# Kernel tuning notes

Hardware: AMD Instinct MI355X
Metric: run time of the kernel (lower is better)

## Reference

```python
import jax, jax.numpy as jnp
import numpy as np

B, S, D, H = 2, 2048, 2048, 16
HD = D // H
QMAX = 127.0  # 8-bit activation quant


def ste_round(x):
    # forward: round; backward: identity
    return x + jax.lax.stop_gradient(jnp.round(x) - x)


def bitlinear(x, w):
    """BitNet b1.58 linear: per-tensor ternary weights + per-token int8 activations.

    x: [..., in], w: [out, in] -> [..., out]
    """
    w_scale = jnp.maximum(jnp.mean(jnp.abs(w)), 1e-6)
    w_q = jnp.clip(ste_round(w / w_scale), -1.0, 1.0)          # ternary {-1,0,1}
    a_max = jnp.clip(jnp.max(jnp.abs(x), axis=-1, keepdims=True), 1e-8, None)
    x_q = jnp.clip(ste_round(x * (QMAX / a_max)), -QMAX, QMAX)  # int8 range
    y = jnp.einsum('bsi,oi->bso', x_q, w_q)
    return y * (w_scale * a_max / QMAX)


def setup_inputs() -> dict:
    key = jax.random.key(0)
    ks = jax.random.split(key, 5)
    std = 1.0 / np.sqrt(D)  # muP-style init from BitLinear
    return {
        'x': jax.random.normal(ks[0], (B, S, D), dtype=jnp.float32),
        'wq': jax.random.normal(ks[1], (D, D), dtype=jnp.float32) * std,
        'wk': jax.random.normal(ks[2], (D, D), dtype=jnp.float32) * std,
        'wv': jax.random.normal(ks[3], (D, D), dtype=jnp.float32) * std,
        'wo': jax.random.normal(ks[4], (D, D), dtype=jnp.float32) * std,
    }


def reference(x, wq, wk, wv, wo):
    q = bitlinear(x, wq).reshape(B, S, H, HD)
    k = bitlinear(x, wk).reshape(B, S, H, HD)
    v = bitlinear(x, wv).reshape(B, S, H, HD)
    scores = jnp.einsum('bqhd,bkhd->bhqk', q, k) / np.sqrt(HD)
    # causal mask
    causal = jnp.tril(jnp.ones((S, S), dtype=bool))
    scores = jnp.where(causal[None, None], scores, jnp.finfo(scores.dtype).min)
    attn = jax.nn.softmax(scores, axis=-1)
    ctx = jnp.einsum('bhqk,bkhd->bqhd', attn, v).reshape(B, S, D)
    return bitlinear(ctx, wo)
```

## Files before the change

kernel.cpp:

```cpp
#include <hip/hip_runtime.h>
#include <hip/hip_bf16.h>
#include <cstdint>
#include <cstddef>


#define BB 2
#define SS 2048
#define DD 2048
#define HH 16
#define HDD 128
#define MM (BB*SS)

typedef __attribute__((ext_vector_type(8))) short bf16x8;
typedef __attribute__((ext_vector_type(4))) float f32x4;
typedef __attribute__((ext_vector_type(16))) float f32x16;
typedef __attribute__((ext_vector_type(4))) int   i32x4;
typedef unsigned short u16;
typedef unsigned int   u32;
typedef unsigned char  u8;
typedef signed char    s8;

#define MFMA(a,b,c)   __builtin_amdgcn_mfma_f32_16x16x32_bf16(a,b,c,0,0,0)
#define MFMA32(a,b,c) __builtin_amdgcn_mfma_f32_32x32x16_bf16(a,b,c,0,0,0)
#define MFMAI8(a,b,c) __builtin_amdgcn_mfma_i32_16x16x64_i8(a,b,c,0,0,0)

static __device__ __forceinline__ u16 f2bf(float f) {
  u32 x = __float_as_uint(f);
  u32 r = x + 0x7fffu + ((x >> 16) & 1u);
  return (u16)(r >> 16);
}

static __device__ __forceinline__ void gl_lds16(const void* g, void* l) {
  __builtin_amdgcn_global_load_lds((const __attribute__((address_space(1))) void*)g,
                                   (__attribute__((address_space(3))) void*)l, 16, 0, 0);
}

__global__ void k_wabs_partial(const float* __restrict__ w0, const float* __restrict__ w1,
                               const float* __restrict__ w2, const float* __restrict__ w3,
                               double* __restrict__ part) {
  int m = blockIdx.x >> 8, blk = blockIdx.x & 255;
  const float* w = (m == 0) ? w0 : (m == 1) ? w1 : (m == 2) ? w2 : w3;
  const float* p = w + (size_t)blk * 16384;
  double s = 0.0;
  for (int i = threadIdx.x * 4; i < 16384; i += 1024) {
    float4 v = *(const float4*)(p + i);
    s += (double)fabsf(v.x) + (double)fabsf(v.y) + (double)fabsf(v.z) + (double)fabsf(v.w);
  }
  __shared__ double red[256];
  red[threadIdx.x] = s;
  __syncthreads();
  for (int off = 128; off > 0; off >>= 1) {
    if ((int)threadIdx.x < off) red[threadIdx.x] += red[threadIdx.x + off];
    __syncthreads();
  }
  if (threadIdx.x == 0) part[m * 256 + blk] = red[0];
}

__global__ void k_wscale_final(const double* __restrict__ part, float* __restrict__ scales) {
  int m = threadIdx.x;
  if (m < 4) {
    double s = 0.0;
    for (int i = 0; i < 256; i++) s += part[m * 256 + i];
    float v = (float)(s * (1.0 / 4194304.0));
    scales[m] = fmaxf(v, 1e-6f);
  }
}

__global__ void k_wquant(const float* __restrict__ w0, const float* __restrict__ w1,
                         const float* __restrict__ w2, const float* __restrict__ w3,
                         s8* __restrict__ wq, const float* __restrict__ scales) {
  int m = blockIdx.y;
  const float* w = (m == 0) ? w0 : (m == 1) ? w1 : (m == 2) ? w2 : w3;
  float ws = scales[m];
  size_t i = ((size_t)blockIdx.x * 256 + threadIdx.x) * 4;
  float4 v = *(const float4*)(w + i);
  s8 o[4];
  o[0] = (s8)(int)fminf(1.f, fmaxf(-1.f, rintf(v.x / ws)));
  o[1] = (s8)(int)fminf(1.f, fmaxf(-1.f, rintf(v.y / ws)));
  o[2] = (s8)(int)fminf(1.f, fmaxf(-1.f, rintf(v.z / ws)));
  o[3] = (s8)(int)fminf(1.f, fmaxf(-1.f, rintf(v.w / ws)));
  *(int*)(wq + (size_t)m * DD * DD + i) = *(const int*)o;
}

__global__ __launch_bounds__(256) void k_rowquant(const float* __restrict__ x, s8* __restrict__ xq,
                                                  float* __restrict__ amax) {
  int row = blockIdx.x, t = threadIdx.x;
  const float* p = x + (size_t)row * DD + t * 8;
  float4 v0 = *(const float4*)(p);
  float4 v1 = *(const float4*)(p + 4);
  float m = fmaxf(fmaxf(fmaxf(fabsf(v0.x), fabsf(v0.y)), fmaxf(fabsf(v0.z), fabsf(v0.w))),
                  fmaxf(fmaxf(fabsf(v1.x), fabsf(v1.y)), fmaxf(fabsf(v1.z), fabsf(v1.w))));
  m = fmaxf(m, __shfl_xor(m, 1));  m = fmaxf(m, __shfl_xor(m, 2));
  m = fmaxf(m, __shfl_xor(m, 4));  m = fmaxf(m, __shfl_xor(m, 8));
  m = fmaxf(m, __shfl_xor(m, 16)); m = fmaxf(m, __shfl_xor(m, 32));
  __shared__ float red[4];
  if ((t & 63) == 0) red[t >> 6] = m;
  __syncthreads();
  m = fmaxf(fmaxf(red[0], red[1]), fmaxf(red[2], red[3]));
  m = fmaxf(m, 1e-8f);
  if (t == 0) amax[row] = m;
  float s = 127.0f / m;
  s8 o[8];
  o[0] = (s8)(int)fminf(127.f, fmaxf(-127.f, rintf(v0.x * s)));
  o[1] = (s8)(int)fminf(127.f, fmaxf(-127.f, rintf(v0.y * s)));
  o[2] = (s8)(int)fminf(127.f, fmaxf(-127.f, rintf(v0.z * s)));
  o[3] = (s8)(int)fminf(127.f, fmaxf(-127.f, rintf(v0.w * s)));
  o[4] = (s8)(int)fminf(127.f, fmaxf(-127.f, rintf(v1.x * s)));
  o[5] = (s8)(int)fminf(127.f, fmaxf(-127.f, rintf(v1.y * s)));
  o[6] = (s8)(int)fminf(127.f, fmaxf(-127.f, rintf(v1.z * s)));
  o[7] = (s8)(int)fminf(127.f, fmaxf(-127.f, rintf(v1.w * s)));
  *(uint2*)(xq + (size_t)row * DD + t * 8) = *(const uint2*)o;
}

template<bool OB, int NBNL>
__global__ __launch_bounds__(512) void k_gemm(const s8* __restrict__ A, const s8* __restrict__ Bw,
                                              const float* __restrict__ amax,
                                              const float* __restrict__ scales, int sbase,
                                              void* __restrict__ outv) {
  __shared__ alignas(16) u8 Asm[2][128 * 128];
  __shared__ alignas(16) u8 Bsm[2][256 * 128];
  int id = blockIdx.x;
  int xcd = id & 7, kk = id >> 3;
  int bm = kk & 31, bn = xcd * NBNL + (kk >> 5);
  int t = threadIdx.x, w = t >> 6, l = t & 63;
  int wr = w >> 2, wc = w & 3;
  int l15 = l & 15, lh = l >> 4;
  int r0 = t >> 3;
  int c0 = ((t & 7) ^ (r0 & 7)) * 16;
  const s8* Ab = A  + (size_t)(bm * 128) * DD;
  const s8* Bb = Bw + (size_t)(bn * 256) * DD;

#define STG_A(tt) do { u8* d_ = &Asm[(tt) & 1][0];                                    \
    gl_lds16(Ab + (size_t)r0 * DD + (tt) * 128 + c0,        d_ + t * 16);             \
    gl_lds16(Ab + (size_t)(r0 + 64) * DD + (tt) * 128 + c0, d_ + (512 + t) * 16); } while (0)
#define STG_B(tt, h_) do { u8* d_ = &Bsm[(tt) & 1][(h_) * 16384];                     \
    gl_lds16(Bb + (size_t)((h_) * 128 + r0) * DD + (tt) * 128 + c0,        d_ + t * 16);\
    gl_lds16(Bb + (size_t)((h_) * 128 + r0 + 64) * DD + (tt) * 128 + c0,   d_ + (512 + t) * 16); } while (0)

  i32x4 acc[4][4] = {};
  STG_A(0); STG_B(0, 0); STG_B(0, 1); STG_B(1, 0);
  asm volatile("s_waitcnt vmcnt(2)" ::: "memory");
  asm volatile("s_barrier" ::: "memory");
  for (int kb = 0; kb < 16; kb++) {
    int b = kb & 1;
    const u8* Ac = &Asm[b][0];
    const u8* Bc = &Bsm[b][0];
    i32x4 af[4][2], bf[2][2];
    #pragma unroll
    for (int i = 0; i < 4; i++)
      #pragma unroll
      for (int ks = 0; ks < 2; ks++)
        af[i][ks] = *(const i32x4*)(Ac + (wr * 64 + i * 16 + l15) * 128 + (((ks * 4 + lh) ^ (l15 & 7)) * 16));
    #pragma unroll
    for (int j = 0; j < 2; j++)
      #pragma unroll
      for (int ks = 0; ks < 2; ks++)
        bf[j][ks] = *(const i32x4*)(Bc + ((wc + 4 * j) * 16 + l15) * 128 + (((ks * 4 + lh) ^ (l15 & 7)) * 16));
    if (kb + 1 < 16) { STG_A(kb + 1); STG_B(kb + 1, 1); }
    asm volatile("s_barrier" ::: "memory");
    asm volatile("s_waitcnt lgkmcnt(0)" ::: "memory");
    __builtin_amdgcn_sched_barrier(0);
    __builtin_amdgcn_s_setprio(1);
    #pragma unroll
    for (int ks = 0; ks < 2; ks++)
      #pragma unroll
      for (int i = 0; i < 4; i++)
        #pragma unroll
        for (int j = 0; j < 2; j++)
          acc[i][j] = MFMAI8(af[i][ks], bf[j][ks], acc[i][j]);
    __builtin_amdgcn_s_setprio(0);
    asm volatile("s_barrier" ::: "memory");
    i32x4 bg[2][2];
    #pragma unroll
    for (int j = 0; j < 2; j++)
      #pragma unroll
      for (int ks = 0; ks < 2; ks++)
        bg[j][ks] = *(const i32x4*)(Bc + ((wc + 4 * (2 + j)) * 16 + l15) * 128 + (((ks * 4 + lh) ^ (l15 & 7)) * 16));
    if (kb + 2 < 16) STG_B(kb + 2, 0);
    asm volatile("s_barrier" ::: "memory");
    asm volatile("s_waitcnt lgkmcnt(0)" ::: "memory");
    __builtin_amdgcn_sched_barrier(0);
    __builtin_amdgcn_s_setprio(1);
    #pragma unroll
    for (int ks = 0; ks < 2; ks++)
      #pragma unroll
      for (int i = 0; i < 4; i++)
        #pragma unroll
        for (int j = 0; j < 2; j++)
          acc[i][2 + j] = MFMAI8(af[i][ks], bg[j][ks], acc[i][2 + j]);
    __builtin_amdgcn_s_setprio(0);
    if (kb < 14) {
      asm volatile("s_waitcnt vmcnt(2)" ::: "memory");
      asm volatile("s_barrier" ::: "memory");
    } else if (kb == 14) {
      asm volatile("s_waitcnt vmcnt(0)" ::: "memory");
      asm volatile("s_barrier" ::: "memory");
    }
  }
#undef STG_A
#undef STG_B
  int mz = OB ? (bn >> 3) : 0;
  int lcol0 = OB ? ((bn & 7) * 256) : (bn * 256);
  float wsc = scales[sbase + mz];
  u16*   outb = (u16*)outv + (size_t)mz * MM * DD;
  float* outf = (float*)outv;
  #pragma unroll
  for (int i = 0; i < 4; i++) {
    int row0 = bm * 128 + wr * 64 + i * 16 + lh * 4;
    #pragma unroll
    for (int r = 0; r < 4; r++) {
      float sc = (wsc * amax[row0 + r]) / 127.0f;
      #pragma unroll
      for (int j = 0; j < 4; j++) {
        int col = lcol0 + (wc + 4 * j) * 16 + l15;
        float y = (float)acc[i][j][r] * sc;
        if (OB) outb[(size_t)(row0 + r) * DD + col] = f2bf(y);
        else    outf[(size_t)(row0 + r) * DD + col] = y;
      }
    }
  }
}

__global__ __launch_bounds__(256) void k_vtrans(const u16* __restrict__ v, u16* __restrict__ vt) {
  __shared__ u16 tile[64][72];
  int sb = blockIdx.x;
  int db = blockIdx.y;
  int bh = blockIdx.z;
  int b = bh >> 4, h = bh & 15;
  int t = threadIdx.x;
  int ls = t >> 2, ld0 = (t & 3) * 16;
  const u16* src = v + (size_t)(b * SS + sb * 64 + ls) * DD + h * HDD + db * 64 + ld0;
  *(int4*)(&tile[ls][ld0])     = *(const int4*)(src);
  *(int4*)(&tile[ls][ld0 + 8]) = *(const int4*)(src + 8);
  __syncthreads();
  int d = t >> 2, s0 = (t & 3) * 16;
  u16 tmp[16];
  #pragma unroll
  for (int k = 0; k < 16; k++) tmp[k] = tile[s0 + k][d];
  u16* dst = vt + (size_t)((bh * HDD) + db * 64 + d) * SS + sb * 64 + s0;
  *(int4*)(dst)     = *(const int4*)(tmp);
  *(int4*)(dst + 8) = *(const int4*)(tmp + 8);
}

__global__ __launch_bounds__(128) void k_attn(const u16* __restrict__ Q, const u16* __restrict__ K,
                                              const u16* __restrict__ VT, float* __restrict__ O) {
  __shared__ u16 Ks[64 * 128];
  __shared__ u16 Vs[128 * 64];
  __shared__ u16 Ps[2 * 32 * 64];
  int id = blockIdx.x;
  int bh = (id & 7) * 4 + ((id >> 3) & 3);
  int qt = 31 - (id >> 5);
  int b = bh >> 4, h = bh & 15;
  int t = threadIdx.x, w = t >> 6, l = t & 63;
  int l31 = l & 31, hi = l >> 5;
  int l15 = l & 15, lh = l >> 4;
  size_t base = (size_t)(b * SS) * DD + h * HDD;
  const u16* vtb = VT + (size_t)bh * HDD * SS;
  u16* Ptw = Ps + w * 2048;
  const float sc  = 0.08838834764831845f;
  const float sc2 = 0.12751944557270094f;
  int ksr[8], kso[8], vsr[8], vso[8];
  #pragma unroll
  for (int i = 0; i < 8; i++) {
    int s = i * 128 + t;
    ksr[i] = s >> 4; kso[i] = ((s & 15) ^ (ksr[i] & 15)) * 8;
    vsr[i] = s >> 3; vso[i] = ((s & 7) ^ (vsr[i] & 7)) * 8;
  }
  int qrow = qt * 64 + w * 32 + l31;
  bf16x8 qf[8];
  #pragma unroll
  for (int kt = 0; kt < 8; kt++)
    qf[kt] = *(const bf16x8*)(Q + base + (size_t)qrow * DD + kt * 16 + hi * 8);
  f32x4 cacc[2][8] = {};
  float mrun = -INFINITY, lrun = 0.f;
  for (int kb = 0; kb <= qt; kb++) {
    #pragma unroll
    for (int i = 0; i < 8; i++)
      gl_lds16(K + base + (size_t)(kb * 64 + ksr[i]) * DD + kso[i], Ks + (i * 128 + t) * 8);
    #pragma unroll
    for (int i = 0; i < 8; i++)
      gl_lds16(vtb + (size_t)vsr[i] * SS + kb * 64 + vso[i], Vs + (i * 128 + t) * 8);
    __syncthreads();
    f32x16 c0 = {}, c1 = {};
    #pragma unroll
    for (int kt = 0; kt < 8; kt++) {
      int sl = (((kt * 2 + hi) ^ (l31 & 15)) * 8);
      bf16x8 kf0 = *(const bf16x8*)(Ks + l31 * 128 + sl);
      bf16x8 kf1 = *(const bf16x8*)(Ks + (32 + l31) * 128 + sl);
      c0 = MFMA32(kf0, qf[kt], c0);
      c1 = MFMA32(kf1, qf[kt], c1);
    }
    if (kb == qt) {
      #pragma unroll
      for (int rg = 0; rg < 16; rg++) {
        int kv0 = kb * 64 + (rg & 3) + 8 * (rg >> 2) + 4 * hi;
        if (kv0 > qrow)      c0[rg] = -1e30f;
        if (kv0 + 32 > qrow) c1[rg] = -1e30f;
      }
    }
    float ta[16];
    #pragma unroll
    for (int rg = 0; rg < 16; rg++) ta[rg] = fmaxf(c0[rg], c1[rg]);
    #pragma unroll
    for (int off = 8; off > 0; off >>= 1)
      #pragma unroll
      for (int rg = 0; rg < 8; rg++)
        if (rg < off) ta[rg] = fmaxf(ta[rg], ta[rg + off]);
    float pmax = fmaxf(ta[0], __shfl_xor(ta[0], 32));
    if (__any(pmax - mrun > 90.50967f)) {
      float mnew = fmaxf(mrun, pmax);
      float alpha = __builtin_amdgcn_exp2f((mrun - mnew) * sc2);
      lrun *= alpha;
      #pragma unroll
      for (int m16 = 0; m16 < 2; m16++)
        #pragma unroll
        for (int r = 0; r < 4; r++) {
          float ar = __shfl(alpha, m16 * 16 + lh * 4 + r);
          #pragma unroll
          for (int n2 = 0; n2 < 8; n2++) cacc[m16][n2][r] *= ar;
        }
      mrun = mnew;
    }
    float msc2 = mrun * sc2;
    float ts[16];
    #pragma unroll
    for (int rg = 0; rg < 16; rg++) {
      float p0 = __builtin_amdgcn_exp2f(fmaf(c0[rg], sc2, -msc2)); c0[rg] = p0;
      float p1 = __builtin_amdgcn_exp2f(fmaf(c1[rg], sc2, -msc2)); c1[rg] = p1;
      ts[rg] = p0 + p1;
    }
    #pragma unroll
    for (int off = 8; off > 0; off >>= 1)
      #pragma unroll
      for (int rg = 0; rg < 8; rg++)
        if (rg < off) ts[rg] += ts[rg + off];
    lrun += ts[0] + __shfl_xor(ts[0], 32);
    #pragma unroll
    for (int q4 = 0; q4 < 4; q4++) {
      uint2 pk0, pk1;
      pk0.x = (u32)f2bf(c0[4 * q4 + 0]) | ((u32)f2bf(c0[4 * q4 + 1]) << 16);
      pk0.y = (u32)f2bf(c0[4 * q4 + 2]) | ((u32)f2bf(c0[4 * q4 + 3]) << 16);
      pk1.x = (u32)f2bf(c1[4 * q4 + 0]) | ((u32)f2bf(c1[4 * q4 + 1]) << 16);
      pk1.y = (u32)f2bf(c1[4 * q4 + 2]) | ((u32)f2bf(c1[4 * q4 + 3]) << 16);
      *(uint2*)(Ptw + l31 * 64 + ((q4 ^ (l31 & 7)) * 8 + 4 * hi))       = pk0;
      *(uint2*)(Ptw + l31 * 64 + (((4 + q4) ^ (l31 & 7)) * 8 + 4 * hi)) = pk1;
    }
    #pragma unroll
    for (int ks = 0; ks < 2; ks++) {
      int so = ((ks * 4 + lh) ^ (l15 & 7)) * 8;
      bf16x8 pf0 = *(const bf16x8*)(Ptw + (l15) * 64 + so);
      bf16x8 pf1 = *(const bf16x8*)(Ptw + (16 + l15) * 64 + so);
      #pragma unroll
      for (int n2 = 0; n2 < 8; n2++) {
        bf16x8 vf = *(const bf16x8*)(Vs + (n2 * 16 + l15) * 64 + so);
        cacc[0][n2] = MFMA(pf0, vf, cacc[0][n2]);
        cacc[1][n2] = MFMA(pf1, vf, cacc[1][n2]);
      }
    }
    __syncthreads();
  }
  float inv = 1.0f / lrun;
  #pragma unroll
  for (int m16 = 0; m16 < 2; m16++)
    #pragma unroll
    for (int r = 0; r < 4; r++) {
      float ir = __shfl(inv, m16 * 16 + lh * 4 + r);
      float* op = O + base + (size_t)(qt * 64 + w * 32 + m16 * 16 + lh * 4 + r) * DD;
      #pragma unroll
      for (int n2 = 0; n2 < 8; n2++)
        op[n2 * 16 + l15] = cacc[m16][n2][r] * ir;
    }
}

extern "C" void kernel_launch(void* const* d_in, const int* in_sizes, int n_in,
                              void* d_out, int out_size, void* d_ws, size_t ws_size,
                              hipStream_t stream) {
  const float* x  = (const float*)d_in[0];
  const float* wq = (const float*)d_in[1];
  const float* wk = (const float*)d_in[2];
  const float* wv = (const float*)d_in[3];
  const float* wo = (const float*)d_in[4];
  char* ws = (char*)d_ws;
  float*  scales = (float*)(ws + 0);
  double* part   = (double*)(ws + 256);
  float*  amaxx  = (float*)(ws + 16384);
  float*  amaxc  = (float*)(ws + 49152);
  s8*     wqq    = (s8*)(ws + 131072);
  s8*     xq     = (s8*)(ws + 33685504);
  u16*    vt16   = (u16*)(ws + 33685504);
  u16*    qb     = (u16*)(ws + 50462720);
  u16*    kb     = (u16*)(ws + 67239936);
  u16*    vb     = (u16*)(ws + 84017152);
  float*  ctx    = (float*)(ws + 100794368);
  (void)in_sizes; (void)n_in; (void)out_size; (void)ws_size;

  k_wabs_partial<<<1024, 256, 0, stream>>>(wq, wk, wv, wo, part);
  k_wscale_final<<<1, 64, 0, stream>>>(part, scales);
  k_wquant<<<dim3(4096, 4), 256, 0, stream>>>(wq, wk, wv, wo, wqq, scales);
  k_rowquant<<<MM, 256, 0, stream>>>(x, xq, amaxx);
  k_gemm<true, 3><<<768, 512, 0, stream>>>(xq, wqq, amaxx, scales, 0, (void*)qb);
  k_vtrans<<<dim3(32, 2, 32), 256, 0, stream>>>(vb, vt16);
  k_attn<<<1024, 128, 0, stream>>>(qb, kb, vt16, ctx);
  k_rowquant<<<MM, 256, 0, stream>>>(ctx, xq, amaxc);
  k_gemm<false, 1><<<256, 512, 0, stream>>>(xq, wqq + (size_t)3 * DD * DD, amaxc, scales, 3, d_out);
}
```

Measured before the change: 232.3 us.

## Double-buffer K/V tiles and pair causal query tiles per attention block

The attention kernel now double-buffers K and V tiles in shared memory, so the next tile's global-to-LDS loads are issued while the current tile is being computed. It also halves the grid, and each block processes a pair of query tiles (pr and 31-pr) so every block does the same amount of causal work. The aim is to hide load latency and balance the triangular workload across blocks. In exchange, LDS use per block roughly doubles, which may cut occupancy, and there are half as many blocks to fill the CUs.

```diff
diff --git a/kernel.cpp b/kernel.cpp
--- a/kernel.cpp
+++ b/kernel.cpp
@@ -244,12 +244,12 @@
 
 __global__ __launch_bounds__(128) void k_attn(const u16* __restrict__ Q, const u16* __restrict__ K,
                                               const u16* __restrict__ VT, float* __restrict__ O) {
-  __shared__ u16 Ks[64 * 128];
-  __shared__ u16 Vs[128 * 64];
-  __shared__ u16 Ps[2 * 32 * 64];
+  __shared__ alignas(16) u16 Ks[2][64 * 128];
+  __shared__ alignas(16) u16 Vs[2][128 * 64];
+  __shared__ alignas(16) u16 Ps[2 * 32 * 64];
   int id = blockIdx.x;
   int bh = (id & 7) * 4 + ((id >> 3) & 3);
-  int qt = 31 - (id >> 5);
+  int pr = id >> 5;
   int b = bh >> 4, h = bh & 15;
   int t = threadIdx.x, w = t >> 6, l = t & 63;
   int l31 = l & 31, hi = l >> 5;
@@ -257,7 +257,6 @@
   size_t base = (size_t)(b * SS) * DD + h * HDD;
   const u16* vtb = VT + (size_t)bh * HDD * SS;
   u16* Ptw = Ps + w * 2048;
-  const float sc  = 0.08838834764831845f;
   const float sc2 = 0.12751944557270094f;
   int ksr[8], kso[8], vsr[8], vso[8];
   #pragma unroll
@@ -266,110 +265,127 @@
     ksr[i] = s >> 4; kso[i] = ((s & 15) ^ (ksr[i] & 15)) * 8;
     vsr[i] = s >> 3; vso[i] = ((s & 7) ^ (vsr[i] & 7)) * 8;
   }
-  int qrow = qt * 64 + w * 32 + l31;
-  bf16x8 qf[8];
-  #pragma unroll
-  for (int kt = 0; kt < 8; kt++)
-    qf[kt] = *(const bf16x8*)(Q + base + (size_t)qrow * DD + kt * 16 + hi * 8);
-  f32x4 cacc[2][8] = {};
-  float mrun = -INFINITY, lrun = 0.f;
-  for (int kb = 0; kb <= qt; kb++) {
-    #pragma unroll
-    for (int i = 0; i < 8; i++)
-      gl_lds16(K + base + (size_t)(kb * 64 + ksr[i]) * DD + kso[i], Ks + (i * 128 + t) * 8);
-    #pragma unroll
-    for (int i = 0; i < 8; i++)
-      gl_lds16(vtb + (size_t)vsr[i] * SS + kb * 64 + vso[i], Vs + (i * 128 + t) * 8);
-    __syncthreads();
-    f32x16 c0 = {}, c1 = {};
-    #pragma unroll
-    for (int kt = 0; kt < 8; kt++) {
-      int sl = (((kt * 2 + hi) ^ (l31 & 15)) * 8);
-      bf16x8 kf0 = *(const bf16x8*)(Ks + l31 * 128 + sl);
-      bf16x8 kf1 = *(const bf16x8*)(Ks + (32 + l31) * 128 + sl);
-      c0 = MFMA32(kf0, qf[kt], c0);
-      c1 = MFMA32(kf1, qf[kt], c1);
+
+#define ASTAGE(kb_, bf_) do {                                                           \
+    _Pragma("unroll")                                                                   \
+    for (int i_ = 0; i_ < 8; i_++)                                                      \
+      gl_lds16(K + base + (size_t)((kb_) * 64 + ksr[i_]) * DD + kso[i_],                \
+               &Ks[bf_][(i_ * 128 + t) * 8]);                                           \
+    _Pragma("unroll")                                                                   \
+    for (int i_ = 0; i_ < 8; i_++)                                                      \
+      gl_lds16(vtb + (size_t)vsr[i_] * SS + (kb_) * 64 + vso[i_],                       \
+               &Vs[bf_][(i_ * 128 + t) * 8]);                                           \
+  } while (0)
+
+  for (int half = 0; half < 2; half++) {
+    int qt = half ? (31 - pr) : pr;
+    int qrow = qt * 64 + w * 32 + l31;
+    bf16x8 qf[8];
+    #pragma unroll
+    for (int kt = 0; kt < 8; kt++)
+      qf[kt] = *(const bf16x8*)(Q + base + (size_t)qrow * DD + kt * 16 + hi * 8);
+    f32x4 cacc[2][8] = {};
+    float mrun = -INFINITY, lrun = 0.f;
+    ASTAGE(0, 0);
+    asm volatile("s_waitcnt vmcnt(0)" ::: "memory");
+    asm volatile("s_barrier" ::: "memory");
+    for (int kb = 0; kb <= qt; kb++) {
+      int cur = kb & 1;
+      if (kb < qt) ASTAGE(kb + 1, cur ^ 1);
+      const u16* Kc = &Ks[cur][0];
+      const u16* Vc = &Vs[cur][0];
+      f32x16 c0 = {}, c1 = {};
+      #pragma unroll
+      for (int kt = 0; kt < 8; kt++) {
+        int sl = (((kt * 2 + hi) ^ (l31 & 15)) * 8);
+        bf16x8 kf0 = *(const bf16x8*)(Kc + l31 * 128 + sl);
+        bf16x8 kf1 = *(const bf16x8*)(Kc + (32 + l31) * 128 + sl);
+        c0 = MFMA32(kf0, qf[kt], c0);
+        c1 = MFMA32(kf1, qf[kt], c1);
+      }
+      if (kb == qt) {
+        #pragma unroll
+        for (int rg = 0; rg < 16; rg++) {
+          int kv0 = kb * 64 + (rg & 3) + 8 * (rg >> 2) + 4 * hi;
+          if (kv0 > qrow)      c0[rg] = -1e30f;
+          if (kv0 + 32 > qrow) c1[rg] = -1e30f;
+        }
+      }
+      float ta[16];
+      #pragma unroll
+      for (int rg = 0; rg < 16; rg++) ta[rg] = fmaxf(c0[rg], c1[rg]);
+      #pragma unroll
+      for (int off = 8; off > 0; off >>= 1)
+        #pragma unroll
+        for (int rg = 0; rg < 8; rg++)
+          if (rg < off) ta[rg] = fmaxf(ta[rg], ta[rg + off]);
+      float pmax = fmaxf(ta[0], __shfl_xor(ta[0], 32));
+      if (__any(pmax - mrun > 90.50967f)) {
+        float mnew = fmaxf(mrun, pmax);
+        float alpha = __builtin_amdgcn_exp2f((mrun - mnew) * sc2);
+        lrun *= alpha;
+        #pragma unroll
+        for (int m16 = 0; m16 < 2; m16++)
+          #pragma unroll
+          for (int r = 0; r < 4; r++) {
+            float ar = __shfl(alpha, m16 * 16 + lh * 4 + r);
+            #pragma unroll
+            for (int n2 = 0; n2 < 8; n2++) cacc[m16][n2][r] *= ar;
+          }
+        mrun = mnew;
+      }
+      float msc2 = mrun * sc2;
+      float ts[16];
+      #pragma unroll
+      for (int rg = 0; rg < 16; rg++) {
+        float p0 = __builtin_amdgcn_exp2f(fmaf(c0[rg], sc2, -msc2)); c0[rg] = p0;
+        float p1 = __builtin_amdgcn_exp2f(fmaf(c1[rg], sc2, -msc2)); c1[rg] = p1;
+        ts[rg] = p0 + p1;
+      }
+      #pragma unroll
+      for (int off = 8; off > 0; off >>= 1)
+        #pragma unroll
+        for (int rg = 0; rg < 8; rg++)
+          if (rg < off) ts[rg] += ts[rg + off];
+      lrun += ts[0] + __shfl_xor(ts[0], 32);
+      #pragma unroll
+      for (int q4 = 0; q4 < 4; q4++) {
+        uint2 pk0, pk1;
+        pk0.x = (u32)f2bf(c0[4 * q4 + 0]) | ((u32)f2bf(c0[4 * q4 + 1]) << 16);
+        pk0.y = (u32)f2bf(c0[4 * q4 + 2]) | ((u32)f2bf(c0[4 * q4 + 3]) << 16);
+        pk1.x = (u32)f2bf(c1[4 * q4 + 0]) | ((u32)f2bf(c1[4 * q4 + 1]) << 16);
+        pk1.y = (u32)f2bf(c1[4 * q4 + 2]) | ((u32)f2bf(c1[4 * q4 + 3]) << 16);
+        *(uint2*)(Ptw + l31 * 64 + ((q4 ^ (l31 & 7)) * 8 + 4 * hi))       = pk0;
+        *(uint2*)(Ptw + l31 * 64 + (((4 + q4) ^ (l31 & 7)) * 8 + 4 * hi)) = pk1;
+      }
+      #pragma unroll
+      for (int ks = 0; ks < 2; ks++) {
+        int so = ((ks * 4 + lh) ^ (l15 & 7)) * 8;
+        bf16x8 pf0 = *(const bf16x8*)(Ptw + (l15) * 64 + so);
+        bf16x8 pf1 = *(const bf16x8*)(Ptw + (16 + l15) * 64 + so);
+        #pragma unroll
+        for (int n2 = 0; n2 < 8; n2++) {
+          bf16x8 vf = *(const bf16x8*)(Vc + (n2 * 16 + l15) * 64 + so);
+          cacc[0][n2] = MFMA(pf0, vf, cacc[0][n2]);
+          cacc[1][n2] = MFMA(pf1, vf, cacc[1][n2]);
+        }
+      }
+      asm volatile("s_waitcnt vmcnt(0)" ::: "memory");
+      asm volatile("s_barrier" ::: "memory");
     }
-    if (kb == qt) {
-      #pragma unroll
-      for (int rg = 0; rg < 16; rg++) {
-        int kv0 = kb * 64 + (rg & 3) + 8 * (rg >> 2) + 4 * hi;
-        if (kv0 > qrow)      c0[rg] = -1e30f;
-        if (kv0 + 32 > qrow) c1[rg] = -1e30f;
-      }
-    }
-    float ta[16];
-    #pragma unroll
-    for (int rg = 0; rg < 16; rg++) ta[rg] = fmaxf(c0[rg], c1[rg]);
-    #pragma unroll
-    for (int off = 8; off > 0; off >>= 1)
-      #pragma unroll
-      for (int rg = 0; rg < 8; rg++)
-        if (rg < off) ta[rg] = fmaxf(ta[rg], ta[rg + off]);
-    float pmax = fmaxf(ta[0], __shfl_xor(ta[0], 32));
-    if (__any(pmax - mrun > 90.50967f)) {
-      float mnew = fmaxf(mrun, pmax);
-      float alpha = __builtin_amdgcn_exp2f((mrun - mnew) * sc2);
-      lrun *= alpha;
-      #pragma unroll
-      for (int m16 = 0; m16 < 2; m16++)
-        #pragma unroll
-        for (int r = 0; r < 4; r++) {
-          float ar = __shfl(alpha, m16 * 16 + lh * 4 + r);
-          #pragma unroll
-          for (int n2 = 0; n2 < 8; n2++) cacc[m16][n2][r] *= ar;
-        }
-      mrun = mnew;
-    }
-    float msc2 = mrun * sc2;
-    float ts[16];
-    #pragma unroll
-    for (int rg = 0; rg < 16; rg++) {
-      float p0 = __builtin_amdgcn_exp2f(fmaf(c0[rg], sc2, -msc2)); c0[rg] = p0;
-      float p1 = __builtin_amdgcn_exp2f(fmaf(c1[rg], sc2, -msc2)); c1[rg] = p1;
-      ts[rg] = p0 + p1;
-    }
-    #pragma unroll
-    for (int off = 8; off > 0; off >>= 1)
-      #pragma unroll
-      for (int rg = 0; rg < 8; rg++)
-        if (rg < off) ts[rg] += ts[rg + off];
-    lrun += ts[0] + __shfl_xor(ts[0], 32);
-    #pragma unroll
-    for (int q4 = 0; q4 < 4; q4++) {
-      uint2 pk0, pk1;
-      pk0.x = (u32)f2bf(c0[4 * q4 + 0]) | ((u32)f2bf(c0[4 * q4 + 1]) << 16);
-      pk0.y = (u32)f2bf(c0[4 * q4 + 2]) | ((u32)f2bf(c0[4 * q4 + 3]) << 16);
-      pk1.x = (u32)f2bf(c1[4 * q4 + 0]) | ((u32)f2bf(c1[4 * q4 + 1]) << 16);
-      pk1.y = (u32)f2bf(c1[4 * q4 + 2]) | ((u32)f2bf(c1[4 * q4 + 3]) << 16);
-      *(uint2*)(Ptw + l31 * 64 + ((q4 ^ (l31 & 7)) * 8 + 4 * hi))       = pk0;
-      *(uint2*)(Ptw + l31 * 64 + (((4 + q4) ^ (l31 & 7)) * 8 + 4 * hi)) = pk1;
-    }
-    #pragma unroll
-    for (int ks = 0; ks < 2; ks++) {
-      int so = ((ks * 4 + lh) ^ (l15 & 7)) * 8;
-      bf16x8 pf0 = *(const bf16x8*)(Ptw + (l15) * 64 + so);
-      bf16x8 pf1 = *(const bf16x8*)(Ptw + (16 + l15) * 64 + so);
-      #pragma unroll
-      for (int n2 = 0; n2 < 8; n2++) {
-        bf16x8 vf = *(const bf16x8*)(Vs + (n2 * 16 + l15) * 64 + so);
-        cacc[0][n2] = MFMA(pf0, vf, cacc[0][n2]);
-        cacc[1][n2] = MFMA(pf1, vf, cacc[1][n2]);
-      }
-    }
-    __syncthreads();
-  }
-  float inv = 1.0f / lrun;
-  #pragma unroll
-  for (int m16 = 0; m16 < 2; m16++)
-    #pragma unroll
-    for (int r = 0; r < 4; r++) {
-      float ir = __shfl(inv, m16 * 16 + lh * 4 + r);
-      float* op = O + base + (size_t)(qt * 64 + w * 32 + m16 * 16 + lh * 4 + r) * DD;
-      #pragma unroll
-      for (int n2 = 0; n2 < 8; n2++)
-        op[n2 * 16 + l15] = cacc[m16][n2][r] * ir;
-    }
+    float inv = 1.0f / lrun;
+    #pragma unroll
+    for (int m16 = 0; m16 < 2; m16++)
+      #pragma unroll
+      for (int r = 0; r < 4; r++) {
+        float ir = __shfl(inv, m16 * 16 + lh * 4 + r);
+        float* op = O + base + (size_t)(qt * 64 + w * 32 + m16 * 16 + lh * 4 + r) * DD;
+        #pragma unroll
+        for (int n2 = 0; n2 < 8; n2++)
+          op[n2 * 16 + l15] = cacc[m16][n2][r] * ir;
+      }
+  }
+#undef ASTAGE
 }
 
 extern "C" void kernel_launch(void* const* d_in, const int* in_sizes, int n_in,
@@ -400,7 +416,7 @@
   k_rowquant<<<MM, 256, 0, stream>>>(x, xq, amaxx);
   k_gemm<true, 3><<<768, 512, 0, stream>>>(xq, wqq, amaxx, scales, 0, (void*)qb);
   k_vtrans<<<dim3(32, 2, 32), 256, 0, stream>>>(vb, vt16);
-  k_attn<<<1024, 128, 0, stream>>>(qb, kb, vt16, ctx);
+  k_attn<<<512, 128, 0, stream>>>(qb, kb, vt16, ctx);
   k_rowquant<<<MM, 256, 0, stream>>>(ctx, xq, amaxc);
   k_gemm<false, 1><<<256, 512, 0, stream>>>(xq, wqq + (size_t)3 * DD * DD, amaxc, scales, 3, d_out);
 }
```

Measured after the change: 236.0 us. No clear change (+1.6%).
